# Kernel tuning notes

Measured on AMD Instinct MI355X. Metric: run time of the kernel, lower is better.

The kernel has to match this reference:

```python
import jax, jax.numpy as jnp
import numpy as np

B, T, H, NI, NO = 128, 2048, 128, 64, 64


def setup_inputs() -> dict:
    key = jax.random.key(0)
    ks = jax.random.split(key, 8)
    sc = 1.0 / np.sqrt(H)

    def p(k, shape):
        return (jax.random.uniform(k, shape, jnp.float32) * 2.0 - 1.0) * sc

    return {
        "X": jax.random.normal(ks[0], (B, T, NI), jnp.float32),
        "h0": jnp.zeros((B, H), jnp.float32),
        # GRUCell params (PyTorch layout: [3H, in] / [3H, H], gate order r,z,n)
        "W_ih": p(ks[1], (3 * H, NI)),
        "W_hh": p(ks[2], (3 * H, H)),
        "b_ih": p(ks[3], (3 * H,)),
        "b_hh": p(ks[4], (3 * H,)),
        # self.W: Linear(H, H, bias=False) applied to h before the cell
        "W_rec": p(ks[5], (H, H)),
        # self.W_out: Linear(H, n_out)
        "W_out": p(ks[6], (NO, H)),
        "b_out": p(ks[7], (NO,)),
    }


def reference(X, h0, W_ih, W_hh, b_ih, b_hh, W_rec, W_out, b_out):
    # Precompute input-gate projections for all timesteps at once: [B,T,3H]
    xg = jnp.einsum("bti,gi->btg", X, W_ih) + b_ih

    def step(h, xg_t):
        hp = h @ W_rec.T                      # W(h), no bias -- fed to GRUCell as hidden
        hg = hp @ W_hh.T + b_hh               # [B,3H]
        xr, xz, xn = jnp.split(xg_t, 3, axis=-1)
        hr, hz, hn = jnpp_split(hg) if False else jnp.split(hg, 3, axis=-1)
        r = jax.nn.sigmoid(xr + hr)
        z = jax.nn.sigmoid(xz + hz)
        n = jnp.tanh(xn + r * hn)
        h_next = (1.0 - z) * n + z * hp       # note: leak term uses W(h), not raw h
        return h_next, h_next

    _, hidden = jax.lax.scan(step, h0, jnp.swapaxes(xg, 0, 1))  # [T,B,H]
    hidden = jnp.swapaxes(hidden, 0, 1)                         # [B,T,H]
    out = hidden @ W_out.T + b_out                              # [B,T,NO]
    return out, hidden
```

## Files before the change

### kernel.cpp

```cpp
#include <hip/hip_runtime.h>

#define B_ 128
#define T_ 2048
#define H_ 128
#define NI_ 64
#define NO_ 64

typedef short s16x8 __attribute__((ext_vector_type(8)));
typedef float f32x4 __attribute__((ext_vector_type(4)));

__device__ __forceinline__ unsigned short f2bf(float f) {
  unsigned int u = __float_as_uint(f);
  u += 0x7fffu + ((u >> 16) & 1u);
  return (unsigned short)(u >> 16);
}
__device__ __forceinline__ f32x4 mfma16(s16x8 a, s16x8 b, f32x4 c) {
  return __builtin_amdgcn_mfma_f32_16x16x32_bf16(a, b, c, 0, 0, 0);
}
__device__ __forceinline__ s16x8 load8(const float* p) {
  float4 a = *reinterpret_cast<const float4*>(p);
  float4 b = *reinterpret_cast<const float4*>(p + 4);
  s16x8 r;
  r[0] = (short)f2bf(a.x); r[1] = (short)f2bf(a.y);
  r[2] = (short)f2bf(a.z); r[3] = (short)f2bf(a.w);
  r[4] = (short)f2bf(b.x); r[5] = (short)f2bf(b.y);
  r[6] = (short)f2bf(b.z); r[7] = (short)f2bf(b.w);
  return r;
}

__global__ __launch_bounds__(512, 2) void gru_seq_kernel(
    const float* __restrict__ X, const float* __restrict__ h0,
    const float* __restrict__ W_ih, const float* __restrict__ W_hh,
    const float* __restrict__ b_ih, const float* __restrict__ b_hh,
    const float* __restrict__ W_rec, const float* __restrict__ W_out,
    const float* __restrict__ b_out,
    float* __restrict__ out, float* __restrict__ hidden)
{
  __shared__ __align__(16) char smem0[34816];
  __shared__ __align__(16) float xnbuf[16][132];
  __shared__ __align__(16) unsigned short hlds[2048];

  auto chunk = reinterpret_cast<unsigned short (*)[136]>(smem0);
  auto ybuf  = reinterpret_cast<float (*)[516]>(smem0);

  const int tid = threadIdx.x;
  const int w   = tid >> 6;
  const int l15 = tid & 15;
  const int lg  = (tid >> 4) & 3;
  const int r0  = blockIdx.x * 16;

  s16x8 bm[4][4];
  if (w < 2) {
    #pragma unroll
    for (int nt = 0; nt < 4; ++nt) {
      int n = 64 * w + 16 * nt + l15;
      #pragma unroll
      for (int kt = 0; kt < 4; ++kt)
        bm[kt][nt] = load8(&W_rec[(size_t)n * H_ + 32 * kt + 8 * lg]);
    }
  }
  for (int c = 0; c < 3; ++c) {
    s16x8 afr[4];
    int m0 = 128 * c + 16 * w;
    #pragma unroll
    for (int kt = 0; kt < 4; ++kt)
      afr[kt] = load8(&W_hh[(size_t)(m0 + l15) * H_ + 32 * kt + 8 * lg]);
    f32x4 D[8];
    #pragma unroll
    for (int nt = 0; nt < 8; ++nt) {
      D[nt] = (f32x4){0.f, 0.f, 0.f, 0.f};
      #pragma unroll
      for (int kt = 0; kt < 4; ++kt) {
        s16x8 bfr;
        int kb = 32 * kt + 8 * lg;
        int n = 16 * nt + l15;
        #pragma unroll
        for (int j = 0; j < 8; ++j)
          bfr[j] = (short)f2bf(W_rec[(size_t)(kb + j) * H_ + n]);
        D[nt] = mfma16(afr[kt], bfr, D[nt]);
      }
    }
    #pragma unroll
    for (int nt = 0; nt < 8; ++nt)
      #pragma unroll
      for (int r = 0; r < 4; ++r)
        chunk[16 * w + 4 * lg + r][16 * nt + l15] = f2bf(D[nt][r]);
    __syncthreads();
    if ((w >> 1) == c + 1) {
      int wl = w & 1;
      #pragma unroll
      for (int nt = 0; nt < 4; ++nt) {
        int cr = 64 * wl + 16 * nt + l15;
        #pragma unroll
        for (int kt = 0; kt < 4; ++kt)
          bm[kt][nt] = *reinterpret_cast<const s16x8*>(&chunk[cr][32 * kt + 8 * lg]);
      }
    }
    __syncthreads();
  }

  s16x8 bw[2][4];
  if (w >= 2) {
    #pragma unroll
    for (int nt = 0; nt < 4; ++nt) {
      int g = 64 * (w - 2) + 16 * nt + l15;
      #pragma unroll
      for (int kt = 0; kt < 2; ++kt)
        bw[kt][nt] = load8(&W_ih[(size_t)g * NI_ + 32 * kt + 8 * lg]);
    }
  }
  s16x8 bo[4];
  float bout = 0.f;
  if (w < 4) {
    int o = 16 * w + l15;
    #pragma unroll
    for (int kt = 0; kt < 4; ++kt)
      bo[kt] = load8(&W_out[(size_t)o * H_ + 32 * kt + 8 * lg]);
    bout = b_out[o];
  }
  float bias[4], biasx[4];
  #pragma unroll
  for (int nt = 0; nt < 4; ++nt) {
    bias[nt] = 0.f; biasx[nt] = 0.f;
    if (w >= 2) {
      int g = 64 * w + 16 * nt + l15 - 128;
      bias[nt] = (w < 6) ? (b_hh[g] + b_ih[g]) : b_hh[g];
      if (w >= 6) biasx[nt] = b_ih[g];
    }
  }
  s16x8 ha[4];
  #pragma unroll
  for (int kt = 0; kt < 4; ++kt)
    ha[kt] = load8(&h0[(size_t)(r0 + l15) * H_ + 32 * kt + 8 * lg]);

  s16x8 xa[2];
  float4 xt[4];
  if (w >= 2) {
    const float* xp = &X[(size_t)(r0 + l15) * T_ * NI_];
    #pragma unroll
    for (int kt = 0; kt < 2; ++kt) {
      xt[2 * kt]     = *reinterpret_cast<const float4*>(xp + 32 * kt + 8 * lg);
      xt[2 * kt + 1] = *reinterpret_cast<const float4*>(xp + 32 * kt + 8 * lg + 4);
    }
    #pragma unroll
    for (int kt = 0; kt < 2; ++kt) {
      float4 a = xt[2 * kt], b = xt[2 * kt + 1];
      s16x8 v;
      v[0]=(short)f2bf(a.x); v[1]=(short)f2bf(a.y); v[2]=(short)f2bf(a.z); v[3]=(short)f2bf(a.w);
      v[4]=(short)f2bf(b.x); v[5]=(short)f2bf(b.y); v[6]=(short)f2bf(b.z); v[7]=(short)f2bf(b.w);
      xa[kt] = v;
    }
  }

  const int row_g = tid >> 5;
  const int j0 = (tid & 31) * 4;
  char* hb = reinterpret_cast<char*>(hlds);

  #pragma unroll 1
  for (int t = 0; t < T_; ++t) {
    if (w >= 2 && t + 1 < T_) {
      const float* xp = &X[((size_t)(r0 + l15) * T_ + (t + 1)) * NI_];
      #pragma unroll
      for (int kt = 0; kt < 2; ++kt) {
        xt[2 * kt]     = *reinterpret_cast<const float4*>(xp + 32 * kt + 8 * lg);
        xt[2 * kt + 1] = *reinterpret_cast<const float4*>(xp + 32 * kt + 8 * lg + 4);
      }
    }
    f32x4 acc[4];
    #pragma unroll
    for (int nt = 0; nt < 4; ++nt)
      acc[nt] = (f32x4){bias[nt], bias[nt], bias[nt], bias[nt]};
    #pragma unroll
    for (int kt = 0; kt < 4; ++kt)
      #pragma unroll
      for (int nt = 0; nt < 4; ++nt)
        acc[nt] = mfma16(ha[kt], bm[kt][nt], acc[nt]);
    f32x4 accx[4];
    if (w >= 2) {
      if (w < 6) {
        #pragma unroll
        for (int kt = 0; kt < 2; ++kt)
          #pragma unroll
          for (int nt = 0; nt < 4; ++nt)
            acc[nt] = mfma16(xa[kt], bw[kt][nt], acc[nt]);
      } else {
        #pragma unroll
        for (int nt = 0; nt < 4; ++nt)
          accx[nt] = (f32x4){biasx[nt], biasx[nt], biasx[nt], biasx[nt]};
        #pragma unroll
        for (int kt = 0; kt < 2; ++kt)
          #pragma unroll
          for (int nt = 0; nt < 4; ++nt)
            accx[nt] = mfma16(xa[kt], bw[kt][nt], accx[nt]);
      }
    }
    if (w < 4 && t > 0) {
      f32x4 ao = (f32x4){0.f, 0.f, 0.f, 0.f};
      #pragma unroll
      for (int kt = 0; kt < 4; ++kt)
        ao = mfma16(ha[kt], bo[kt], ao);
      #pragma unroll
      for (int r = 0; r < 4; ++r)
        out[((size_t)(r0 + 4 * lg + r) * T_ + (t - 1)) * NO_ + 16 * w + l15] = ao[r] + bout;
    }
    #pragma unroll
    for (int nt = 0; nt < 4; ++nt)
      #pragma unroll
      for (int r = 0; r < 4; ++r)
        ybuf[4 * lg + r][64 * w + 16 * nt + l15] = acc[nt][r];
    if (w >= 6)
      #pragma unroll
      for (int nt = 0; nt < 4; ++nt)
        #pragma unroll
        for (int r = 0; r < 4; ++r)
          xnbuf[4 * lg + r][64 * (w - 6) + 16 * nt + l15] = accx[nt][r];
    __syncthreads();

    float4 vhp = *reinterpret_cast<const float4*>(&ybuf[row_g][j0]);
    float4 vr  = *reinterpret_cast<const float4*>(&ybuf[row_g][128 + j0]);
    float4 vz  = *reinterpret_cast<const float4*>(&ybuf[row_g][256 + j0]);
    float4 vnh = *reinterpret_cast<const float4*>(&ybuf[row_g][384 + j0]);
    float4 vnx = *reinterpret_cast<const float4*>(&xnbuf[row_g][j0]);
    float hp[4] = {vhp.x, vhp.y, vhp.z, vhp.w};
    float pr[4] = {vr.x, vr.y, vr.z, vr.w};
    float pz[4] = {vz.x, vz.y, vz.z, vz.w};
    float nh[4] = {vnh.x, vnh.y, vnh.z, vnh.w};
    float nx[4] = {vnx.x, vnx.y, vnx.z, vnx.w};
    float hn[4];
    #pragma unroll
    for (int q = 0; q < 4; ++q) {
      float rg = 1.f / (1.f + __expf(-pr[q]));
      float zg = 1.f / (1.f + __expf(-pz[q]));
      float a2 = nx[q] + rg * nh[q];
      float e2 = __expf(2.f * a2);
      float ng = (e2 - 1.f) / (e2 + 1.f);
      hn[q] = (1.f - zg) * ng + zg * hp[q];
    }
    *reinterpret_cast<float4*>(&hidden[((size_t)(r0 + row_g) * T_ + t) * H_ + j0]) =
        make_float4(hn[0], hn[1], hn[2], hn[3]);
    {
      int ktj = j0 >> 5, lgj = (j0 >> 3) & 3, ej = j0 & 7;
      unsigned int idx = (unsigned)((ktj * 4 + lgj) * 256 + row_g * 16 + ej * 2);
      idx ^= ((idx >> 8) & 7u) << 4;
      unsigned int p0 = (unsigned)f2bf(hn[0]) | ((unsigned)f2bf(hn[1]) << 16);
      unsigned int p1 = (unsigned)f2bf(hn[2]) | ((unsigned)f2bf(hn[3]) << 16);
      *reinterpret_cast<uint2*>(hb + idx) = make_uint2(p0, p1);
    }
    __syncthreads();
    #pragma unroll
    for (int kt = 0; kt < 4; ++kt) {
      unsigned int idx = (unsigned)((kt * 4 + lg) * 256 + l15 * 16);
      idx ^= ((idx >> 8) & 7u) << 4;
      ha[kt] = *reinterpret_cast<const s16x8*>(hb + idx);
    }
    if (w >= 2 && t + 1 < T_) {
      #pragma unroll
      for (int kt = 0; kt < 2; ++kt) {
        float4 a = xt[2 * kt], b = xt[2 * kt + 1];
        s16x8 v;
        v[0]=(short)f2bf(a.x); v[1]=(short)f2bf(a.y); v[2]=(short)f2bf(a.z); v[3]=(short)f2bf(a.w);
        v[4]=(short)f2bf(b.x); v[5]=(short)f2bf(b.y); v[6]=(short)f2bf(b.z); v[7]=(short)f2bf(b.w);
        xa[kt] = v;
      }
    }
  }
  if (w < 4) {
    f32x4 ao = (f32x4){0.f, 0.f, 0.f, 0.f};
    #pragma unroll
    for (int kt = 0; kt < 4; ++kt)
      ao = mfma16(ha[kt], bo[kt], ao);
    #pragma unroll
    for (int r = 0; r < 4; ++r)
      out[((size_t)(r0 + 4 * lg + r) * T_ + (T_ - 1)) * NO_ + 16 * w + l15] = ao[r] + bout;
  }
}

extern "C" void kernel_launch(void* const* d_in, const int* in_sizes, int n_in,
                              void* d_out, int out_size, void* d_ws, size_t ws_size,
                              hipStream_t stream) {
  const float* X     = (const float*)d_in[0];
  const float* h0    = (const float*)d_in[1];
  const float* W_ih  = (const float*)d_in[2];
  const float* W_hh  = (const float*)d_in[3];
  const float* b_ih  = (const float*)d_in[4];
  const float* b_hh  = (const float*)d_in[5];
  const float* W_rec = (const float*)d_in[6];
  const float* W_out = (const float*)d_in[7];
  const float* b_out = (const float*)d_in[8];
  float* out    = (float*)d_out;
  float* hidden = out + (size_t)B_ * T_ * NO_;
  gru_seq_kernel<<<dim3(8), dim3(512), 0, stream>>>(X, h0, W_ih, W_hh, b_ih, b_hh,
                                                    W_rec, W_out, b_out, out, hidden);
}
```

Baseline: 6.411 ms.

## Transpose recurrent GEMM so each wave owns hidden slice, drop ybuf LDS exchange

Switches the per-step MFMA so weights are the A operand and h is the B operand. Each wave now computes hp, r, z, n_h and n_x for its own 16-column hidden slice, so the gate nonlinearity runs directly on accumulators without staging through ybuf/xnbuf. This removes one __syncthreads and a large LDS write/read per timestep. It also double-buffers the h LDS buffer, vectorizes out/hidden stores, and spreads the x-projection across all waves, at the cost of more weight registers per wave.

```diff
diff --git a/kernel.cpp b/kernel.cpp
--- a/kernel.cpp
+++ b/kernel.cpp
@@ -27,6 +27,14 @@
   r[6] = (short)f2bf(b.z); r[7] = (short)f2bf(b.w);
   return r;
 }
+__device__ __forceinline__ s16x8 cvt8(float4 a, float4 b) {
+  s16x8 v;
+  v[0] = (short)f2bf(a.x); v[1] = (short)f2bf(a.y);
+  v[2] = (short)f2bf(a.z); v[3] = (short)f2bf(a.w);
+  v[4] = (short)f2bf(b.x); v[5] = (short)f2bf(b.y);
+  v[6] = (short)f2bf(b.z); v[7] = (short)f2bf(b.w);
+  return v;
+}
 
 __global__ __launch_bounds__(512, 2) void gru_seq_kernel(
     const float* __restrict__ X, const float* __restrict__ h0,
@@ -36,12 +44,8 @@
     const float* __restrict__ b_out,
     float* __restrict__ out, float* __restrict__ hidden)
 {
-  __shared__ __align__(16) char smem0[34816];
-  __shared__ __align__(16) float xnbuf[16][132];
-  __shared__ __align__(16) unsigned short hlds[2048];
-
-  auto chunk = reinterpret_cast<unsigned short (*)[136]>(smem0);
-  auto ybuf  = reinterpret_cast<float (*)[516]>(smem0);
+  __shared__ __align__(16) unsigned short chunk[128][136];
+  __shared__ __align__(16) unsigned short hlds[2][2048];
 
   const int tid = threadIdx.x;
   const int w   = tid >> 6;
@@ -49,22 +53,17 @@
   const int lg  = (tid >> 4) & 3;
   const int r0  = blockIdx.x * 16;
 
-  s16x8 bm[4][4];
-  if (w < 2) {
-    #pragma unroll
-    for (int nt = 0; nt < 4; ++nt) {
-      int n = 64 * w + 16 * nt + l15;
-      #pragma unroll
-      for (int kt = 0; kt < 4; ++kt)
-        bm[kt][nt] = load8(&W_rec[(size_t)n * H_ + 32 * kt + 8 * lg]);
-    }
-  }
+  s16x8 am_hp[4];
+  #pragma unroll
+  for (int kt = 0; kt < 4; ++kt)
+    am_hp[kt] = load8(&W_rec[(size_t)(16 * w + l15) * H_ + 32 * kt + 8 * lg]);
+
+  s16x8 am_g[3][4];
   for (int c = 0; c < 3; ++c) {
     s16x8 afr[4];
-    int m0 = 128 * c + 16 * w;
-    #pragma unroll
-    for (int kt = 0; kt < 4; ++kt)
-      afr[kt] = load8(&W_hh[(size_t)(m0 + l15) * H_ + 32 * kt + 8 * lg]);
+    #pragma unroll
+    for (int kt = 0; kt < 4; ++kt)
+      afr[kt] = load8(&W_hh[(size_t)(128 * c + 16 * w + l15) * H_ + 32 * kt + 8 * lg]);
     f32x4 D[8];
     #pragma unroll
     for (int nt = 0; nt < 8; ++nt) {
@@ -72,8 +71,7 @@
       #pragma unroll
       for (int kt = 0; kt < 4; ++kt) {
         s16x8 bfr;
-        int kb = 32 * kt + 8 * lg;
-        int n = 16 * nt + l15;
+        int kb = 32 * kt + 8 * lg, n = 16 * nt + l15;
         #pragma unroll
         for (int j = 0; j < 8; ++j)
           bfr[j] = (short)f2bf(W_rec[(size_t)(kb + j) * H_ + n]);
@@ -86,192 +84,131 @@
       for (int r = 0; r < 4; ++r)
         chunk[16 * w + 4 * lg + r][16 * nt + l15] = f2bf(D[nt][r]);
     __syncthreads();
-    if ((w >> 1) == c + 1) {
-      int wl = w & 1;
-      #pragma unroll
-      for (int nt = 0; nt < 4; ++nt) {
-        int cr = 64 * wl + 16 * nt + l15;
-        #pragma unroll
-        for (int kt = 0; kt < 4; ++kt)
-          bm[kt][nt] = *reinterpret_cast<const s16x8*>(&chunk[cr][32 * kt + 8 * lg]);
-      }
-    }
+    #pragma unroll
+    for (int kt = 0; kt < 4; ++kt)
+      am_g[c][kt] = *reinterpret_cast<const s16x8*>(&chunk[16 * w + l15][32 * kt + 8 * lg]);
     __syncthreads();
   }
 
-  s16x8 bw[2][4];
-  if (w >= 2) {
-    #pragma unroll
-    for (int nt = 0; nt < 4; ++nt) {
-      int g = 64 * (w - 2) + 16 * nt + l15;
-      #pragma unroll
-      for (int kt = 0; kt < 2; ++kt)
-        bw[kt][nt] = load8(&W_ih[(size_t)g * NI_ + 32 * kt + 8 * lg]);
-    }
-  }
-  s16x8 bo[4];
-  float bout = 0.f;
+  s16x8 ax_g[3][2];
+  #pragma unroll
+  for (int g = 0; g < 3; ++g)
+    #pragma unroll
+    for (int kt = 0; kt < 2; ++kt)
+      ax_g[g][kt] = load8(&W_ih[(size_t)(128 * g + 16 * w + l15) * NI_ + 32 * kt + 8 * lg]);
+
+  s16x8 ao[4];
+  f32x4 bo = (f32x4){0.f, 0.f, 0.f, 0.f};
   if (w < 4) {
-    int o = 16 * w + l15;
-    #pragma unroll
-    for (int kt = 0; kt < 4; ++kt)
-      bo[kt] = load8(&W_out[(size_t)o * H_ + 32 * kt + 8 * lg]);
-    bout = b_out[o];
-  }
-  float bias[4], biasx[4];
-  #pragma unroll
-  for (int nt = 0; nt < 4; ++nt) {
-    bias[nt] = 0.f; biasx[nt] = 0.f;
-    if (w >= 2) {
-      int g = 64 * w + 16 * nt + l15 - 128;
-      bias[nt] = (w < 6) ? (b_hh[g] + b_ih[g]) : b_hh[g];
-      if (w >= 6) biasx[nt] = b_ih[g];
-    }
-  }
+    #pragma unroll
+    for (int kt = 0; kt < 4; ++kt)
+      ao[kt] = load8(&W_out[(size_t)(16 * w + l15) * H_ + 32 * kt + 8 * lg]);
+    #pragma unroll
+    for (int r = 0; r < 4; ++r)
+      bo[r] = b_out[16 * w + 4 * lg + r];
+  }
+
+  f32x4 br, bz, bnh, bnx;
+  #pragma unroll
+  for (int r = 0; r < 4; ++r) {
+    int d = 16 * w + 4 * lg + r;
+    br[r]  = b_ih[d] + b_hh[d];
+    bz[r]  = b_ih[H_ + d] + b_hh[H_ + d];
+    bnx[r] = b_ih[2 * H_ + d];
+    bnh[r] = b_hh[2 * H_ + d];
+  }
+
   s16x8 ha[4];
   #pragma unroll
   for (int kt = 0; kt < 4; ++kt)
     ha[kt] = load8(&h0[(size_t)(r0 + l15) * H_ + 32 * kt + 8 * lg]);
 
-  s16x8 xa[2];
+  const float* xptr = &X[(size_t)(r0 + l15) * T_ * NI_];
+  const float* xpf  = xptr + NI_;
   float4 xt[4];
-  if (w >= 2) {
-    const float* xp = &X[(size_t)(r0 + l15) * T_ * NI_];
-    #pragma unroll
-    for (int kt = 0; kt < 2; ++kt) {
-      xt[2 * kt]     = *reinterpret_cast<const float4*>(xp + 32 * kt + 8 * lg);
-      xt[2 * kt + 1] = *reinterpret_cast<const float4*>(xp + 32 * kt + 8 * lg + 4);
-    }
-    #pragma unroll
-    for (int kt = 0; kt < 2; ++kt) {
-      float4 a = xt[2 * kt], b = xt[2 * kt + 1];
-      s16x8 v;
-      v[0]=(short)f2bf(a.x); v[1]=(short)f2bf(a.y); v[2]=(short)f2bf(a.z); v[3]=(short)f2bf(a.w);
-      v[4]=(short)f2bf(b.x); v[5]=(short)f2bf(b.y); v[6]=(short)f2bf(b.z); v[7]=(short)f2bf(b.w);
-      xa[kt] = v;
-    }
-  }
-
-  const int row_g = tid >> 5;
-  const int j0 = (tid & 31) * 4;
-  char* hb = reinterpret_cast<char*>(hlds);
+  s16x8 xb[2];
+  #pragma unroll
+  for (int kt = 0; kt < 2; ++kt) {
+    xt[2 * kt]     = *reinterpret_cast<const float4*>(xptr + 32 * kt + 8 * lg);
+    xt[2 * kt + 1] = *reinterpret_cast<const float4*>(xptr + 32 * kt + 8 * lg + 4);
+  }
+  #pragma unroll
+  for (int kt = 0; kt < 2; ++kt)
+    xb[kt] = cvt8(xt[2 * kt], xt[2 * kt + 1]);
+
+  float* hidp = hidden + (size_t)(r0 + l15) * T_ * H_ + 16 * w + 4 * lg;
+  float* outp = out + (size_t)(r0 + l15) * T_ * NO_ + 16 * w + 4 * lg;
+  char* hbase = reinterpret_cast<char*>(hlds);
+  const unsigned int wsw = (unsigned)(l15 & 7) << 4;
+  const unsigned int waddr = ((unsigned)(l15 * 256 + (16 * w + 4 * lg) * 2)) ^ wsw;
 
   #pragma unroll 1
   for (int t = 0; t < T_; ++t) {
-    if (w >= 2 && t + 1 < T_) {
-      const float* xp = &X[((size_t)(r0 + l15) * T_ + (t + 1)) * NI_];
+    if (t + 1 < T_) {
       #pragma unroll
       for (int kt = 0; kt < 2; ++kt) {
-        xt[2 * kt]     = *reinterpret_cast<const float4*>(xp + 32 * kt + 8 * lg);
-        xt[2 * kt + 1] = *reinterpret_cast<const float4*>(xp + 32 * kt + 8 * lg + 4);
+        xt[2 * kt]     = *reinterpret_cast<const float4*>(xpf + 32 * kt + 8 * lg);
+        xt[2 * kt + 1] = *reinterpret_cast<const float4*>(xpf + 32 * kt + 8 * lg + 4);
       }
-    }
-    f32x4 acc[4];
-    #pragma unroll
-    for (int nt = 0; nt < 4; ++nt)
-      acc[nt] = (f32x4){bias[nt], bias[nt], bias[nt], bias[nt]};
-    #pragma unroll
-    for (int kt = 0; kt < 4; ++kt)
-      #pragma unroll
-      for (int nt = 0; nt < 4; ++nt)
-        acc[nt] = mfma16(ha[kt], bm[kt][nt], acc[nt]);
-    f32x4 accx[4];
-    if (w >= 2) {
-      if (w < 6) {
-        #pragma unroll
-        for (int kt = 0; kt < 2; ++kt)
-          #pragma unroll
-          for (int nt = 0; nt < 4; ++nt)
-            acc[nt] = mfma16(xa[kt], bw[kt][nt], acc[nt]);
-      } else {
-        #pragma unroll
-        for (int nt = 0; nt < 4; ++nt)
-          accx[nt] = (f32x4){biasx[nt], biasx[nt], biasx[nt], biasx[nt]};
-        #pragma unroll
-        for (int kt = 0; kt < 2; ++kt)
-          #pragma unroll
-          for (int nt = 0; nt < 4; ++nt)
-            accx[nt] = mfma16(xa[kt], bw[kt][nt], accx[nt]);
-      }
+      xpf += NI_;
     }
     if (w < 4 && t > 0) {
-      f32x4 ao = (f32x4){0.f, 0.f, 0.f, 0.f};
+      f32x4 oa = bo;
       #pragma unroll
       for (int kt = 0; kt < 4; ++kt)
-        ao = mfma16(ha[kt], bo[kt], ao);
-      #pragma unroll
-      for (int r = 0; r < 4; ++r)
-        out[((size_t)(r0 + 4 * lg + r) * T_ + (t - 1)) * NO_ + 16 * w + l15] = ao[r] + bout;
-    }
-    #pragma unroll
-    for (int nt = 0; nt < 4; ++nt)
-      #pragma unroll
-      for (int r = 0; r < 4; ++r)
-        ybuf[4 * lg + r][64 * w + 16 * nt + l15] = acc[nt][r];
-    if (w >= 6)
-      #pragma unroll
-      for (int nt = 0; nt < 4; ++nt)
-        #pragma unroll
-        for (int r = 0; r < 4; ++r)
-          xnbuf[4 * lg + r][64 * (w - 6) + 16 * nt + l15] = accx[nt][r];
-    __syncthreads();
-
-    float4 vhp = *reinterpret_cast<const float4*>(&ybuf[row_g][j0]);
-    float4 vr  = *reinterpret_cast<const float4*>(&ybuf[row_g][128 + j0]);
-    float4 vz  = *reinterpret_cast<const float4*>(&ybuf[row_g][256 + j0]);
-    float4 vnh = *reinterpret_cast<const float4*>(&ybuf[row_g][384 + j0]);
-    float4 vnx = *reinterpret_cast<const float4*>(&xnbuf[row_g][j0]);
-    float hp[4] = {vhp.x, vhp.y, vhp.z, vhp.w};
-    float pr[4] = {vr.x, vr.y, vr.z, vr.w};
-    float pz[4] = {vz.x, vz.y, vz.z, vz.w};
-    float nh[4] = {vnh.x, vnh.y, vnh.z, vnh.w};
-    float nx[4] = {vnx.x, vnx.y, vnx.z, vnx.w};
+        oa = mfma16(ao[kt], ha[kt], oa);
+      *reinterpret_cast<float4*>(outp) = make_float4(oa[0], oa[1], oa[2], oa[3]);
+      outp += NO_;
+    }
+    f32x4 ahp = (f32x4){0.f, 0.f, 0.f, 0.f};
+    f32x4 ar = br, az = bz, anh = bnh, anx = bnx;
+    #pragma unroll
+    for (int kt = 0; kt < 4; ++kt) {
+      ahp = mfma16(am_hp[kt],   ha[kt], ahp);
+      ar  = mfma16(am_g[0][kt], ha[kt], ar);
+      az  = mfma16(am_g[1][kt], ha[kt], az);
+      anh = mfma16(am_g[2][kt], ha[kt], anh);
+    }
+    #pragma unroll
+    for (int kt = 0; kt < 2; ++kt) {
+      ar  = mfma16(ax_g[0][kt], xb[kt], ar);
+      az  = mfma16(ax_g[1][kt], xb[kt], az);
+      anx = mfma16(ax_g[2][kt], xb[kt], anx);
+    }
     float hn[4];
     #pragma unroll
     for (int q = 0; q < 4; ++q) {
-      float rg = 1.f / (1.f + __expf(-pr[q]));
-      float zg = 1.f / (1.f + __expf(-pz[q]));
-      float a2 = nx[q] + rg * nh[q];
+      float rg = 1.f / (1.f + __expf(-ar[q]));
+      float zg = 1.f / (1.f + __expf(-az[q]));
+      float a2 = anx[q] + rg * anh[q];
       float e2 = __expf(2.f * a2);
       float ng = (e2 - 1.f) / (e2 + 1.f);
-      hn[q] = (1.f - zg) * ng + zg * hp[q];
-    }
-    *reinterpret_cast<float4*>(&hidden[((size_t)(r0 + row_g) * T_ + t) * H_ + j0]) =
-        make_float4(hn[0], hn[1], hn[2], hn[3]);
-    {
-      int ktj = j0 >> 5, lgj = (j0 >> 3) & 3, ej = j0 & 7;
-      unsigned int idx = (unsigned)((ktj * 4 + lgj) * 256 + row_g * 16 + ej * 2);
-      idx ^= ((idx >> 8) & 7u) << 4;
-      unsigned int p0 = (unsigned)f2bf(hn[0]) | ((unsigned)f2bf(hn[1]) << 16);
-      unsigned int p1 = (unsigned)f2bf(hn[2]) | ((unsigned)f2bf(hn[3]) << 16);
-      *reinterpret_cast<uint2*>(hb + idx) = make_uint2(p0, p1);
+      hn[q] = (1.f - zg) * ng + zg * ahp[q];
+    }
+    *reinterpret_cast<float4*>(hidp) = make_float4(hn[0], hn[1], hn[2], hn[3]);
+    hidp += H_;
+    unsigned int p0 = (unsigned)f2bf(hn[0]) | ((unsigned)f2bf(hn[1]) << 16);
+    unsigned int p1 = (unsigned)f2bf(hn[2]) | ((unsigned)f2bf(hn[3]) << 16);
+    char* hb = hbase + ((t & 1) << 12);
+    *reinterpret_cast<uint2*>(hb + waddr) = make_uint2(p0, p1);
+    if (t + 1 < T_) {
+      #pragma unroll
+      for (int kt = 0; kt < 2; ++kt)
+        xb[kt] = cvt8(xt[2 * kt], xt[2 * kt + 1]);
     }
     __syncthreads();
     #pragma unroll
     for (int kt = 0; kt < 4; ++kt) {
-      unsigned int idx = (unsigned)((kt * 4 + lg) * 256 + l15 * 16);
-      idx ^= ((idx >> 8) & 7u) << 4;
-      ha[kt] = *reinterpret_cast<const s16x8*>(hb + idx);
-    }
-    if (w >= 2 && t + 1 < T_) {
-      #pragma unroll
-      for (int kt = 0; kt < 2; ++kt) {
-        float4 a = xt[2 * kt], b = xt[2 * kt + 1];
-        s16x8 v;
-        v[0]=(short)f2bf(a.x); v[1]=(short)f2bf(a.y); v[2]=(short)f2bf(a.z); v[3]=(short)f2bf(a.w);
-        v[4]=(short)f2bf(b.x); v[5]=(short)f2bf(b.y); v[6]=(short)f2bf(b.z); v[7]=(short)f2bf(b.w);
-        xa[kt] = v;
-      }
+      unsigned int ra = ((unsigned)(l15 * 256 + 64 * kt + 16 * lg)) ^ wsw;
+      ha[kt] = *reinterpret_cast<const s16x8*>(hb + ra);
     }
   }
   if (w < 4) {
-    f32x4 ao = (f32x4){0.f, 0.f, 0.f, 0.f};
-    #pragma unroll
-    for (int kt = 0; kt < 4; ++kt)
-      ao = mfma16(ha[kt], bo[kt], ao);
-    #pragma unroll
-    for (int r = 0; r < 4; ++r)
-      out[((size_t)(r0 + 4 * lg + r) * T_ + (T_ - 1)) * NO_ + 16 * w + l15] = ao[r] + bout;
+    f32x4 oa = bo;
+    #pragma unroll
+    for (int kt = 0; kt < 4; ++kt)
+      oa = mfma16(ao[kt], ha[kt], oa);
+    *reinterpret_cast<float4*>(outp) = make_float4(oa[0], oa[1], oa[2], oa[3]);
   }
 }
 
```

After: 9.715 ms. 1.52x slower.
